# Kernel optimization log

Measured on AMD Instinct MI355X. Metric: run time of the kernel, lower is better.

The kernel has to match this reference:

```python
import jax, jax.numpy as jnp
import numpy as np

GAMMA, ZETA = -0.1, 1.1
N_BITS = 4
QMAX = (1 << N_BITS) - 1  # 15
OUT, IN, D, K = 4096, 4096, 8, 4096
L = (OUT * IN) // D  # 2097152 blocks, no padding needed


def setup_inputs() -> dict:
    key = jax.random.key(0)
    k = jax.random.split(key, 7)
    x = jax.random.normal(k[0], (4, 2048, IN), jnp.float32)
    codebook = jax.random.normal(k[1], (K, D), jnp.float32)
    indices = jax.random.randint(k[2], (L,), 0, K, jnp.int32)
    base_int = jax.random.randint(k[3], (OUT, IN), 0, QMAX, jnp.int32)
    scale = jax.random.uniform(k[4], (OUT, 1), jnp.float32)
    zero = jax.random.uniform(k[5], (OUT, 1), jnp.float32)
    bias = jax.random.normal(k[6], (OUT,), jnp.float32)
    return {"x": x, "codebook": codebook, "indices": indices,
            "base_int": base_int, "scale": scale, "zero": zero, "bias": bias}


def reference(x, codebook, indices, base_int, scale, zero, bias):
    # Gather codebook blocks and rebuild alpha with the weight's shape [OUT, IN]
    alpha = codebook[indices].reshape(OUT, IN)
    # Rectified sigmoid (soft quant mode)
    r = jnp.clip(jax.nn.sigmoid(alpha) * (ZETA - GAMMA) + GAMMA, 0.0, 1.0)
    # Affine int-quant reconstruction
    q_int = jnp.clip(base_int.astype(scale.dtype) + r + zero, 0.0, float(QMAX))
    Wq = scale * (q_int - zero)  # [OUT, IN]
    # F.linear: x @ Wq^T + bias
    return jnp.einsum('bsi,oi->bso', x, Wq) + bias
```

## Files before the change

kernel.cpp:

```cpp
#include <hip/hip_runtime.h>

#define M_DIM 8192
#define N_DIM 4096
#define K_DIM 4096
#define L_BLK 2097152
#define K2 8192

typedef __attribute__((ext_vector_type(8))) short short8;
typedef __attribute__((ext_vector_type(8))) unsigned short ushort8;
typedef __attribute__((ext_vector_type(4))) float f32x4;

__device__ __forceinline__ unsigned short f2bf(float f) {
  unsigned int u = __float_as_uint(f);
  unsigned int r = (u + 0x7fffu + ((u >> 16) & 1u)) >> 16;
  return (unsigned short)r;
}

__device__ __forceinline__ void gld16(const void* g, void* l) {
  __builtin_amdgcn_global_load_lds(
      (const __attribute__((address_space(1))) void*)g,
      (__attribute__((address_space(3))) void*)l, 16, 0, 0);
}

__global__ void dequant_kernel(const float* __restrict__ cb,
                               const int* __restrict__ idx,
                               const int* __restrict__ base,
                               const float* __restrict__ scale,
                               const float* __restrict__ zero,
                               unsigned short* __restrict__ W) {
  const int b = blockIdx.x * 256 + threadIdx.x;
  const int o = b >> 9;
  const float s = scale[o];
  const float z = zero[o];
  const int ci = idx[b];
  const float4* crow = (const float4*)(cb + (size_t)ci * 8);
  float4 c0 = crow[0], c1 = crow[1];
  const int4* brow = (const int4*)(base + (size_t)b * 8);
  int4 b0 = brow[0], b1 = brow[1];
  float a[8]  = {c0.x, c0.y, c0.z, c0.w, c1.x, c1.y, c1.z, c1.w};
  int   bi[8] = {b0.x, b0.y, b0.z, b0.w, b1.x, b1.y, b1.z, b1.w};
  union { unsigned short h[8]; ushort8 v; } u;
#pragma unroll
  for (int d = 0; d < 8; ++d) {
    float sg = 1.0f / (1.0f + __expf(-a[d]));
    float r = fminf(fmaxf(sg * 1.2f - 0.1f, 0.0f), 1.0f);
    float q = fminf(fmaxf((float)bi[d] + r + z, 0.0f), 15.0f);
    u.h[d] = f2bf(s * (q - z));
  }
  *(ushort8*)(W + (size_t)b * 8) = u.v;
}

__global__ void xconv_kernel(const float* __restrict__ x,
                             unsigned short* __restrict__ xb) {
  const size_t i = (size_t)blockIdx.x * 256 + threadIdx.x;
  const float4* X = (const float4*)x;
  float4 a0 = X[i * 2], a1 = X[i * 2 + 1];
  float f[8] = {a0.x, a0.y, a0.z, a0.w, a1.x, a1.y, a1.z, a1.w};
  union { unsigned short h[8]; ushort8 v; } u;
#pragma unroll
  for (int d = 0; d < 8; ++d) u.h[d] = f2bf(f[d]);
  *(ushort8*)(xb + i * 8) = u.v;
}


#define BAR __builtin_amdgcn_s_barrier()
#define LGKM0 do { asm volatile("s_waitcnt lgkmcnt(0)" ::: "memory"); \
                   __builtin_amdgcn_sched_barrier(0); } while (0)
#define VMW(N) asm volatile("s_waitcnt vmcnt(" #N ")" ::: "memory")

#define RD_B_ALL(BUFO) \
  _Pragma("unroll") for (int n = 0; n < 4; ++n) \
  _Pragma("unroll") for (int kk = 0; kk < 2; ++kk) \
    bf[n][kk] = *(const short8*)(lds + (BUFO) + 32768 + \
        (wn * 64 + n * 16 + r16) * 128 + (acol0 ^ (kk << 6)));

#define RD_A_PAIR(BUFO, P) \
  _Pragma("unroll") for (int mi = 0; mi < 2; ++mi) \
  _Pragma("unroll") for (int kk = 0; kk < 2; ++kk) \
    af[mi][kk] = *(const short8*)(lds + (BUFO) + \
        (wm * 128 + (2 * (P) + mi) * 16 + r16) * 128 + (acol0 ^ (kk << 6)));

#define MFMA_PAIR(P) do { \
  __builtin_amdgcn_s_setprio(1); \
  _Pragma("unroll") for (int kk = 0; kk < 2; ++kk) \
  _Pragma("unroll") for (int mi = 0; mi < 2; ++mi) \
  _Pragma("unroll") for (int n = 0; n < 4; ++n) \
    acc[2 * (P) + mi][n] = __builtin_amdgcn_mfma_f32_16x16x32_bf16( \
        af[mi][kk], bf[n][kk], acc[2 * (P) + mi][n], 0, 0, 0); \
  __builtin_amdgcn_s_setprio(0); \
} while (0)

__global__ __launch_bounds__(512, 2)
void gemm_bt(const unsigned short* __restrict__ A,
             const unsigned short* __restrict__ B,
             const float* __restrict__ bias,
             float* __restrict__ C) {
  __shared__ char lds[131072];
  const int tid = threadIdx.x;
  const int lane = tid & 63;
  const int w = tid >> 6;
  const int wm = w >> 2;
  const int wn = w & 3;
  const int r16 = lane & 15;
  const int g = lane >> 4;
  const int swr = (r16 & 7) << 4;
  const int acol0 = (g << 4) ^ swr;

  const int s = (int)blockIdx.x;
  const int wg = (s & 7) * 64 + (s >> 3);
  const int bm = wg & 31;
  const int bn = wg >> 5;

  const char* Abase = (const char*)A + (size_t)bm * 256 * K2;
  const char* Bbase = (const char*)B + (size_t)bn * 256 * K2;

  const int strow = tid >> 3;
  const int scol = ((tid & 7) * 16) ^ ((strow & 7) << 4);
  const int sdst = w * 1024;

  auto stA = [&](int bo, int c, int kt) {
    gld16(Abase + (size_t)(c * 64 + strow) * K2 + kt * 128 + scol,
          lds + bo + c * 8192 + sdst);
  };
  auto stB = [&](int bo, int c, int kt) {
    gld16(Bbase + (size_t)(c * 64 + strow) * K2 + kt * 128 + scol,
          lds + bo + 32768 + c * 8192 + sdst);
  };

  f32x4 acc[8][4] = {};
  short8 bf[4][2];
  short8 af[2][2];

  stB(0, 0, 0); stB(0, 1, 0); stB(0, 2, 0); stB(0, 3, 0);
  stA(0, 0, 0); stA(0, 1, 0); stA(0, 2, 0); stA(0, 3, 0);
  VMW(0);
  BAR;

  int bufo = 0;
  for (int t = 0; t < 63; ++t) {
    const int nxt = bufo ^ 65536;
    const int kt = t + 1;
    RD_B_ALL(bufo); RD_A_PAIR(bufo, 0);
    stB(nxt, 0, kt); stB(nxt, 1, kt);
    BAR; LGKM0; MFMA_PAIR(0); BAR;
    RD_A_PAIR(bufo, 1);
    stB(nxt, 2, kt); stB(nxt, 3, kt);
    VMW(4);
    BAR; LGKM0; MFMA_PAIR(1); BAR;
    RD_A_PAIR(bufo, 2);
    stA(nxt, 0, kt); stA(nxt, 2, kt);
    BAR; LGKM0; MFMA_PAIR(2); BAR;
    RD_A_PAIR(bufo, 3);
    stA(nxt, 1, kt); stA(nxt, 3, kt);
    VMW(2);
    BAR; LGKM0; MFMA_PAIR(3); BAR;
    bufo = nxt;
  }
  RD_B_ALL(bufo); RD_A_PAIR(bufo, 0);
  BAR; LGKM0; MFMA_PAIR(0); BAR;
  RD_A_PAIR(bufo, 1);
  VMW(0);
  BAR; LGKM0; MFMA_PAIR(1); BAR;
  RD_A_PAIR(bufo, 2);
  BAR; LGKM0; MFMA_PAIR(2); BAR;
  RD_A_PAIR(bufo, 3);
  BAR; LGKM0; MFMA_PAIR(3); BAR;

  const int cb0 = bn * 256 + wn * 64 + r16;
  float bv[4];
#pragma unroll
  for (int n = 0; n < 4; ++n) bv[n] = bias[cb0 + n * 16];
#pragma unroll
  for (int m = 0; m < 8; ++m) {
#pragma unroll
    for (int j = 0; j < 4; ++j) {
      int row = bm * 256 + wm * 128 + m * 16 + g * 4 + j;
      float* Crow = C + (size_t)row * N_DIM + cb0;
#pragma unroll
      for (int n = 0; n < 4; ++n) Crow[n * 16] = acc[m][n][j] + bv[n];
    }
  }
}

extern "C" void kernel_launch(void* const* d_in, const int* in_sizes, int n_in,
                              void* d_out, int out_size, void* d_ws, size_t ws_size,
                              hipStream_t stream) {
  const float* x     = (const float*)d_in[0];
  const float* cb    = (const float*)d_in[1];
  const int*   idx   = (const int*)d_in[2];
  const int*   base  = (const int*)d_in[3];
  const float* scale = (const float*)d_in[4];
  const float* zero  = (const float*)d_in[5];
  const float* bias  = (const float*)d_in[6];
  float* out = (float*)d_out;

  unsigned short* Wq = (unsigned short*)d_ws;
  unsigned short* Xb = (unsigned short*)((char*)d_ws + (size_t)N_DIM * K_DIM * 2);

  dequant_kernel<<<L_BLK / 256, 256, 0, stream>>>(cb, idx, base, scale, zero, Wq);
  xconv_kernel<<<(M_DIM * K_DIM / 8) / 256, 256, 0, stream>>>(x, Xb);
  gemm_bt<<<(M_DIM / 256) * (N_DIM / 256), 512, 0, stream>>>(Xb, Wq, bias, out);
}
```

Baseline: 322.3 us.

## Software-pipeline LDS fragment reads with double-buffered registers and fewer barriers

The GEMM main loop now double-buffers A and B fragments in registers, so the LDS reads for the next MFMA group are issued while the current group computes. The explicit lgkmcnt(0) waits are replaced by compiler-managed waits behind sched_barrier fences. Barriers per K-tile drop from eight to three, and global loads are regrouped into 6+2 batches. This is meant to hide LDS latency and barrier stalls, at the cost of more VGPRs, which could cut occupancy at 2 waves/SIMD, and with ordering now relying on compiler waitcnt insertion.

```diff
diff --git a/kernel.cpp b/kernel.cpp
--- a/kernel.cpp
+++ b/kernel.cpp
@@ -63,31 +63,48 @@
 }
 
 
-#define BAR __builtin_amdgcn_s_barrier()
-#define LGKM0 do { asm volatile("s_waitcnt lgkmcnt(0)" ::: "memory"); \
-                   __builtin_amdgcn_sched_barrier(0); } while (0)
 #define VMW(N) asm volatile("s_waitcnt vmcnt(" #N ")" ::: "memory")
-
-#define RD_B_ALL(BUFO) \
+#define FENCE asm volatile("" ::: "memory")
+#define BARM do { FENCE; __builtin_amdgcn_s_barrier(); FENCE; } while (0)
+
+#define RDB(BF, BUFO) \
   _Pragma("unroll") for (int n = 0; n < 4; ++n) \
   _Pragma("unroll") for (int kk = 0; kk < 2; ++kk) \
-    bf[n][kk] = *(const short8*)(lds + (BUFO) + 32768 + \
+    BF[n][kk] = *(const short8*)(lds + (BUFO) + 32768 + \
         (wn * 64 + n * 16 + r16) * 128 + (acol0 ^ (kk << 6)));
 
-#define RD_A_PAIR(BUFO, P) \
+#define RDA(AF, BUFO, P) \
   _Pragma("unroll") for (int mi = 0; mi < 2; ++mi) \
   _Pragma("unroll") for (int kk = 0; kk < 2; ++kk) \
-    af[mi][kk] = *(const short8*)(lds + (BUFO) + \
+    AF[mi][kk] = *(const short8*)(lds + (BUFO) + \
         (wm * 128 + (2 * (P) + mi) * 16 + r16) * 128 + (acol0 ^ (kk << 6)));
 
-#define MFMA_PAIR(P) do { \
+#define FMQ(P, AF, BF) do { \
   __builtin_amdgcn_s_setprio(1); \
+  __builtin_amdgcn_sched_barrier(0); \
   _Pragma("unroll") for (int kk = 0; kk < 2; ++kk) \
   _Pragma("unroll") for (int mi = 0; mi < 2; ++mi) \
   _Pragma("unroll") for (int n = 0; n < 4; ++n) \
     acc[2 * (P) + mi][n] = __builtin_amdgcn_mfma_f32_16x16x32_bf16( \
-        af[mi][kk], bf[n][kk], acc[2 * (P) + mi][n], 0, 0, 0); \
+        AF[mi][kk], BF[n][kk], acc[2 * (P) + mi][n], 0, 0, 0); \
+  __builtin_amdgcn_sched_barrier(0); \
   __builtin_amdgcn_s_setprio(0); \
+} while (0)
+
+#define STAGE6(NXT, KT) do { \
+  stB(NXT, 0, KT); stB(NXT, 1, KT); stB(NXT, 2, KT); stB(NXT, 3, KT); \
+  stA(NXT, 0, KT); stA(NXT, 2, KT); } while (0)
+#define STAGE2(NXT, KT) do { stA(NXT, 1, KT); stA(NXT, 3, KT); } while (0)
+
+#define ITER(BFC, BFN, CUR, NXT, KT) do { \
+   \
+  RDA(afB, CUR, 1); STAGE6(NXT, KT); FMQ(0, afA, BFC); VMW(6); BARM; \
+   \
+  RDA(afA, CUR, 2); STAGE2(NXT, KT); FMQ(1, afB, BFC); \
+   \
+  RDA(afB, CUR, 3); FMQ(2, afA, BFC); VMW(2); BARM; \
+   \
+  RDB(BFN, NXT); RDA(afA, NXT, 0); FMQ(3, afB, BFC); BARM; \
 } while (0)
 
 __global__ __launch_bounds__(512, 2)
@@ -103,8 +120,7 @@
   const int wn = w & 3;
   const int r16 = lane & 15;
   const int g = lane >> 4;
-  const int swr = (r16 & 7) << 4;
-  const int acol0 = (g << 4) ^ swr;
+  const int acol0 = (g << 4) ^ ((r16 & 7) << 4);
 
   const int s = (int)blockIdx.x;
   const int wg = (s & 7) * 64 + (s >> 3);
@@ -128,43 +144,24 @@
   };
 
   f32x4 acc[8][4] = {};
-  short8 bf[4][2];
-  short8 af[2][2];
-
-  stB(0, 0, 0); stB(0, 1, 0); stB(0, 2, 0); stB(0, 3, 0);
-  stA(0, 0, 0); stA(0, 1, 0); stA(0, 2, 0); stA(0, 3, 0);
-  VMW(0);
-  BAR;
-
-  int bufo = 0;
-  for (int t = 0; t < 63; ++t) {
-    const int nxt = bufo ^ 65536;
-    const int kt = t + 1;
-    RD_B_ALL(bufo); RD_A_PAIR(bufo, 0);
-    stB(nxt, 0, kt); stB(nxt, 1, kt);
-    BAR; LGKM0; MFMA_PAIR(0); BAR;
-    RD_A_PAIR(bufo, 1);
-    stB(nxt, 2, kt); stB(nxt, 3, kt);
-    VMW(4);
-    BAR; LGKM0; MFMA_PAIR(1); BAR;
-    RD_A_PAIR(bufo, 2);
-    stA(nxt, 0, kt); stA(nxt, 2, kt);
-    BAR; LGKM0; MFMA_PAIR(2); BAR;
-    RD_A_PAIR(bufo, 3);
-    stA(nxt, 1, kt); stA(nxt, 3, kt);
-    VMW(2);
-    BAR; LGKM0; MFMA_PAIR(3); BAR;
-    bufo = nxt;
+  short8 bfA[4][2], bfB[4][2];
+  short8 afA[2][2], afB[2][2];
+
+  STAGE6(0, 0); STAGE2(0, 0);
+  VMW(0); BARM;
+  RDB(bfA, 0); RDA(afA, 0, 0);
+
+  for (int tp = 0; tp < 31; ++tp) {
+    ITER(bfA, bfB, 0, 65536, 2 * tp + 1);
+    ITER(bfB, bfA, 65536, 0, 2 * tp + 2);
   }
-  RD_B_ALL(bufo); RD_A_PAIR(bufo, 0);
-  BAR; LGKM0; MFMA_PAIR(0); BAR;
-  RD_A_PAIR(bufo, 1);
-  VMW(0);
-  BAR; LGKM0; MFMA_PAIR(1); BAR;
-  RD_A_PAIR(bufo, 2);
-  BAR; LGKM0; MFMA_PAIR(2); BAR;
-  RD_A_PAIR(bufo, 3);
-  BAR; LGKM0; MFMA_PAIR(3); BAR;
+  ITER(bfA, bfB, 0, 65536, 63);
+  RDA(afB, 65536, 1); FMQ(0, afA, bfB); VMW(0); BARM;
+  RDA(afA, 65536, 2); FMQ(1, afB, bfB);
+  RDA(afB, 65536, 3); FMQ(2, afA, bfB);
+  FMQ(3, afB, bfB);
+
+  FENCE;
 
   const int cb0 = bn * 256 + wn * 64 + r16;
   float bv[4];
```

Measured after the change: 331.8 us. 2.9% more time.
